# Kernel tuning notes

Hardware: AMD Instinct MI355X
Metric: run time of the kernel (lower is better)

The kernel has to match this reference:

```python
import jax, jax.numpy as jnp
import numpy as np

H, I, E, TOP_K = 2048, 1408, 16, 6
IS = 2816  # shared-expert intermediate = moe_intermediate_size * n_shared_experts
NORM_TOPK_PROB = False


def _silu_and_mul(gate_up):
    # gate_up: [..., 2*I] -> silu(gate) * up, [..., I]
    d = gate_up.shape[-1] // 2
    g, u = gate_up[..., :d], gate_up[..., d:]
    return jax.nn.silu(g) * u


def setup_inputs() -> dict:
    key = jax.random.key(0)
    ks = jax.random.split(key, 6)
    s = 0.02
    return {
        "x": jax.random.normal(ks[0], (1, 2048, H), jnp.float32),
        "gate_w": jax.random.normal(ks[1], (E, H), jnp.float32) * s,
        "w1": jax.random.normal(ks[2], (E, 2 * I, H), jnp.float32) * s,
        "w2": jax.random.normal(ks[3], (E, H, I), jnp.float32) * s,
        "shared_w1": jax.random.normal(ks[4], (2 * IS, H), jnp.float32) * s,
        "shared_w2": jax.random.normal(ks[5], (H, IS), jnp.float32) * s,
    }


def reference(x, gate_w, w1, w2, shared_w1, shared_w2):
    B, S, Hd = x.shape
    xf = x.reshape(-1, Hd)  # [T, H]
    T = xf.shape[0]

    # shared experts (dense MLP over all tokens)
    shared_out = _silu_and_mul(xf @ shared_w1.T) @ shared_w2.T  # [T, H]

    # router: softmax in fp32, then top-k
    logits = xf @ gate_w.T  # [T, E]
    probs = jax.nn.softmax(logits.astype(jnp.float32), axis=-1)
    routing_weights, selected = jax.lax.top_k(probs, TOP_K)  # [T, k]
    if NORM_TOPK_PROB:
        routing_weights = routing_weights / routing_weights.sum(-1, keepdims=True)

    # scatter top-k weights into dense [T, E] combine matrix (fused_moe equivalent)
    combine = jnp.zeros((T, E), jnp.float32).at[
        jnp.arange(T)[:, None], selected
    ].add(routing_weights).astype(x.dtype)

    # expert MLPs, combined with routing weights
    gate_up = jnp.einsum('th,eoh->teo', xf, w1)  # [T, E, 2I]
    act = _silu_and_mul(gate_up)                 # [T, E, I]
    moe_out = jnp.einsum('te,tei,ehi->th', combine, act, w2)  # [T, H]

    return (moe_out + shared_out).reshape(B, S, Hd)
```

## Files before the change

kernel.cpp:

```cpp
#include <hip/hip_runtime.h>
#include <hip/hip_bf16.h>
#include <cstdint>
#include <cstddef>


typedef __bf16 bf16;
typedef __bf16 bf16x8 __attribute__((ext_vector_type(8)));
typedef float  f32x4  __attribute__((ext_vector_type(4)));

constexpr int Hdim  = 2048;
constexpr int Idim  = 1408;
constexpr int NE    = 16;
constexpr int TOPK  = 6;
constexpr int ISdim = 2816;
constexpr int Ttok  = 2048;
constexpr int BMG   = 256;
constexpr int MAX_SLOTS = 16384;

__device__ __forceinline__ void gll16(const void* g, void* l) {
  __builtin_amdgcn_global_load_lds((__attribute__((address_space(1))) void*)(g),
                                   (__attribute__((address_space(3))) void*)(l),
                                   16, 0, 0);
}


__global__ void init_kernel(int* cnt, int* fill, int* tok_of_slot, float* wt_of_slot) {
  int i = blockIdx.x * 256 + threadIdx.x;
  if (i < NE) { cnt[i] = 0; fill[i] = 0; }
  if (i < MAX_SLOTS) { tok_of_slot[i] = -1; wt_of_slot[i] = 0.f; }
}

__global__ void cvt_kernel(const float* __restrict__ src, bf16* __restrict__ dst, int n8) {
  int i = blockIdx.x * 256 + threadIdx.x;
  if (i >= n8) return;
  f32x4 f0 = *(const f32x4*)(src + (size_t)i * 8);
  f32x4 f1 = *(const f32x4*)(src + (size_t)i * 8 + 4);
  bf16x8 v;
#pragma unroll
  for (int j = 0; j < 4; j++) { v[j] = (bf16)f0[j]; v[j + 4] = (bf16)f1[j]; }
  *(bf16x8*)(dst + (size_t)i * 8) = v;
}

__global__ void router_kernel(const float* __restrict__ x, const float* __restrict__ gw,
                              int* __restrict__ sel_e, float* __restrict__ sel_w,
                              int* __restrict__ cnt) {
  int t = blockIdx.x;
  int lane = threadIdx.x;
  const float* xr = x + (size_t)t * Hdim;
  float acc[NE];
#pragma unroll
  for (int e = 0; e < NE; e++) acc[e] = 0.f;
  for (int h = lane; h < Hdim; h += 64) {
    float xv = xr[h];
#pragma unroll
    for (int e = 0; e < NE; e++) acc[e] += xv * gw[e * Hdim + h];
  }
#pragma unroll
  for (int e = 0; e < NE; e++) {
#pragma unroll
    for (int off = 32; off > 0; off >>= 1) acc[e] += __shfl_xor(acc[e], off, 64);
  }
  if (lane == 0) {
    float m = acc[0];
#pragma unroll
    for (int e = 1; e < NE; e++) m = fmaxf(m, acc[e]);
    float p[NE]; float s = 0.f;
#pragma unroll
    for (int e = 0; e < NE; e++) { p[e] = __expf(acc[e] - m); s += p[e]; }
    float inv = 1.f / s;
    bool used[NE];
#pragma unroll
    for (int e = 0; e < NE; e++) used[e] = false;
    for (int k = 0; k < TOPK; k++) {
      int best = 0; float bv = -1.f;
      for (int e = 0; e < NE; e++) if (!used[e] && p[e] > bv) { bv = p[e]; best = e; }
      used[best] = true;
      sel_e[t * TOPK + k] = best;
      sel_w[t * TOPK + k] = bv * inv;
      atomicAdd(&cnt[best], 1);
    }
  }
}

__global__ void scan_kernel(const int* __restrict__ cnt, int* __restrict__ pbase,
                            int* __restrict__ mtiles) {
  if (threadIdx.x == 0 && blockIdx.x == 0) {
    int pb = 0;
    for (int e = 0; e < NE; e++) {
      pbase[e] = pb;
      int mt = (cnt[e] + BMG - 1) / BMG;
      mtiles[e] = mt;
      pb += mt * BMG;
    }
  }
}

__global__ void assign_kernel(const int* __restrict__ sel_e, const float* __restrict__ sel_w,
                              const int* __restrict__ pbase, int* __restrict__ fill,
                              int* __restrict__ tok_of_slot, float* __restrict__ wt_of_slot) {
  int i = blockIdx.x * 256 + threadIdx.x;
  if (i >= Ttok * TOPK) return;
  int t = i / TOPK;
  int e = sel_e[i];
  int pos = atomicAdd(&fill[e], 1);
  int slot = pbase[e] + pos;
  tok_of_slot[slot] = t;
  wt_of_slot[slot] = sel_w[i];
}


template <bool GROUPED, bool BF16B, int BM>
__global__ __launch_bounds__(256, 2)
void gateup_kernel(const bf16* __restrict__ Abase, const void* __restrict__ Wv,
                   bf16* __restrict__ Cact,
                   const int* __restrict__ tok_of_slot, const float* __restrict__ wt_of_slot,
                   const int* __restrict__ pbase, const int* __restrict__ mtiles,
                   int K, int Isz) {
  constexpr int NQ = BM / 64;
  constexpr int WROWS = BM / 4;
  constexpr int NI = WROWS / 16;
  const int e = GROUPED ? blockIdx.z : 0;
  const int mt = blockIdx.y;
  if (GROUPED) { if (mt >= mtiles[e]) return; }
  const int row0 = (GROUPED ? pbase[e] : 0) + mt * BM;
  const int col0 = blockIdx.x * 64;
  const int tid = threadIdx.x;
  const int lane = tid & 63;
  const int wv = tid >> 6;
  const int m16 = lane & 15, quad = lane >> 4;

  __shared__ __align__(16) bf16 ldsA[BM * 32];
  __shared__ __align__(16) bf16 ldsG[64 * 32];
  __shared__ __align__(16) bf16 ldsU[64 * 32];

  const int srow = tid >> 2;
  const int scol = (tid & 3) * 8;

  const bf16* aptr[NQ];
#pragma unroll
  for (int q = 0; q < NQ; q++) {
    int r = row0 + q * 64 + srow;
    int tok = GROUPED ? tok_of_slot[r] : r;
    if (GROUPED && tok < 0) tok = 0;
    aptr[q] = Abase + (size_t)tok * K + scol;
  }

  const bf16* gptrB = nullptr; const bf16* uptrB = nullptr;
  const float* GrowF = nullptr; const float* UrowF = nullptr;
  f32x4 gb0, gb1, ub0, ub1;
  if constexpr (BF16B) {
    const bf16* Wb = (const bf16*)Wv + (size_t)e * 2 * Isz * K;
    gptrB = Wb + (size_t)(col0 + srow) * K + scol;
    uptrB = Wb + (size_t)(Isz + col0 + srow) * K + scol;
  } else {
    const float* Wb = (const float*)Wv + (size_t)e * 2 * Isz * K;
    GrowF = Wb + (size_t)(col0 + srow) * K + scol;
    UrowF = Wb + (size_t)(Isz + col0 + srow) * K + scol;
    gb0 = *(const f32x4*)(GrowF);
    gb1 = *(const f32x4*)(GrowF + 4);
    ub0 = *(const f32x4*)(UrowF);
    ub1 = *(const f32x4*)(UrowF + 4);
  }

  f32x4 accg[NI][4], accu[NI][4];
#pragma unroll
  for (int i = 0; i < NI; i++)
#pragma unroll
    for (int j = 0; j < 4; j++)
#pragma unroll
      for (int r = 0; r < 4; r++) { accg[i][j][r] = 0.f; accu[i][j][r] = 0.f; }

  for (int k0 = 0; k0 < K; k0 += 32) {
    if constexpr (BF16B) {
      gll16(gptrB + k0, &ldsG[tid * 8]);
      gll16(uptrB + k0, &ldsU[tid * 8]);
    } else {
      bf16x8 gv, uv;
#pragma unroll
      for (int j = 0; j < 4; j++) {
        gv[j] = (bf16)gb0[j]; gv[j + 4] = (bf16)gb1[j];
        uv[j] = (bf16)ub0[j]; uv[j + 4] = (bf16)ub1[j];
      }
      *(bf16x8*)(&ldsG[tid * 8]) = gv;
      *(bf16x8*)(&ldsU[tid * 8]) = uv;
      if (k0 + 32 < K) {
        gb0 = *(const f32x4*)(GrowF + k0 + 32);
        gb1 = *(const f32x4*)(GrowF + k0 + 36);
        ub0 = *(const f32x4*)(UrowF + k0 + 32);
        ub1 = *(const f32x4*)(UrowF + k0 + 36);
      }
    }
#pragma unroll
    for (int q = 0; q < NQ; q++) gll16(aptr[q] + k0, &ldsA[q * 2048 + tid * 8]);
    __syncthreads();
    bf16x8 af[NI], gf[4], uf[4];
#pragma unroll
    for (int i = 0; i < NI; i++)
      af[i] = *(const bf16x8*)(&ldsA[(wv * WROWS + i * 16 + m16) * 32 + quad * 8]);
#pragma unroll
    for (int j = 0; j < 4; j++) {
      gf[j] = *(const bf16x8*)(&ldsG[(j * 16 + m16) * 32 + quad * 8]);
      uf[j] = *(const bf16x8*)(&ldsU[(j * 16 + m16) * 32 + quad * 8]);
    }
#pragma unroll
    for (int i = 0; i < NI; i++)
#pragma unroll
      for (int j = 0; j < 4; j++) {
        accg[i][j] = __builtin_amdgcn_mfma_f32_16x16x32_bf16(af[i], gf[j], accg[i][j], 0, 0, 0);
        accu[i][j] = __builtin_amdgcn_mfma_f32_16x16x32_bf16(af[i], uf[j], accu[i][j], 0, 0, 0);
      }
    __syncthreads();
  }

#pragma unroll
  for (int i = 0; i < NI; i++) {
#pragma unroll
    for (int r = 0; r < 4; r++) {
      int grow = row0 + wv * WROWS + i * 16 + quad * 4 + r;
      float scale = 1.f;
      if (GROUPED) scale = wt_of_slot[grow];
#pragma unroll
      for (int j = 0; j < 4; j++) {
        float g = accg[i][j][r];
        float u = accu[i][j][r];
        float a = g * u * scale / (1.f + __expf(-g));
        Cact[(size_t)grow * Isz + (col0 + j * 16 + m16)] = (bf16)a;
      }
    }
  }
}


template <bool GROUPED, bool BF16B, int BM>
__global__ __launch_bounds__(256, 2)
void down_kernel(const bf16* __restrict__ A, const void* __restrict__ Wv,
                 float* __restrict__ out, const int* __restrict__ tok_of_slot,
                 const int* __restrict__ pbase, const int* __restrict__ mtiles, int K) {
  constexpr int NQ = BM / 64;
  constexpr int WROWS = BM / 4;
  constexpr int NI = WROWS / 16;
  const int e = GROUPED ? blockIdx.z : 0;
  const int mt = blockIdx.y;
  if (GROUPED) { if (mt >= mtiles[e]) return; }
  const int row0 = (GROUPED ? pbase[e] : 0) + mt * BM;
  const int col0 = blockIdx.x * 128;
  const int tid = threadIdx.x;
  const int lane = tid & 63;
  const int wv = tid >> 6;
  const int m16 = lane & 15, quad = lane >> 4;

  __shared__ __align__(16) bf16 ldsA[BM * 32];
  __shared__ __align__(16) bf16 ldsB[128 * 32];

  const int srow = tid >> 2;
  const int scol = (tid & 3) * 8;

  const bf16* aptr[NQ];
#pragma unroll
  for (int q = 0; q < NQ; q++)
    aptr[q] = A + (size_t)(row0 + q * 64 + srow) * K + scol;

  const bf16* bptrB[2] = {nullptr, nullptr};
  const float* BrowF[2] = {nullptr, nullptr};
  f32x4 bb[2][2];
  if constexpr (BF16B) {
    const bf16* Wb = (const bf16*)Wv + (size_t)e * Hdim * K;
#pragma unroll
    for (int q = 0; q < 2; q++)
      bptrB[q] = Wb + (size_t)(col0 + q * 64 + srow) * K + scol;
  } else {
    const float* Wb = (const float*)Wv + (size_t)e * Hdim * K;
#pragma unroll
    for (int q = 0; q < 2; q++) {
      BrowF[q] = Wb + (size_t)(col0 + q * 64 + srow) * K + scol;
      bb[q][0] = *(const f32x4*)(BrowF[q]);
      bb[q][1] = *(const f32x4*)(BrowF[q] + 4);
    }
  }

  f32x4 acc[NI][8];
#pragma unroll
  for (int i = 0; i < NI; i++)
#pragma unroll
    for (int j = 0; j < 8; j++)
#pragma unroll
      for (int r = 0; r < 4; r++) acc[i][j][r] = 0.f;

  for (int k0 = 0; k0 < K; k0 += 32) {
    if constexpr (BF16B) {
#pragma unroll
      for (int q = 0; q < 2; q++) gll16(bptrB[q] + k0, &ldsB[q * 2048 + tid * 8]);
    } else {
#pragma unroll
      for (int q = 0; q < 2; q++) {
        bf16x8 bv;
#pragma unroll
        for (int j = 0; j < 4; j++) { bv[j] = (bf16)bb[q][0][j]; bv[j + 4] = (bf16)bb[q][1][j]; }
        *(bf16x8*)(&ldsB[q * 2048 + tid * 8]) = bv;
      }
      if (k0 + 32 < K) {
#pragma unroll
        for (int q = 0; q < 2; q++) {
          bb[q][0] = *(const f32x4*)(BrowF[q] + k0 + 32);
          bb[q][1] = *(const f32x4*)(BrowF[q] + k0 + 36);
        }
      }
    }
#pragma unroll
    for (int q = 0; q < NQ; q++) gll16(aptr[q] + k0, &ldsA[q * 2048 + tid * 8]);
    __syncthreads();
    bf16x8 af[NI], bfr[8];
#pragma unroll
    for (int i = 0; i < NI; i++)
      af[i] = *(const bf16x8*)(&ldsA[(wv * WROWS + i * 16 + m16) * 32 + quad * 8]);
#pragma unroll
    for (int j = 0; j < 8; j++)
      bfr[j] = *(const bf16x8*)(&ldsB[(j * 16 + m16) * 32 + quad * 8]);
#pragma unroll
    for (int i = 0; i < NI; i++)
#pragma unroll
      for (int j = 0; j < 8; j++)
        acc[i][j] = __builtin_amdgcn_mfma_f32_16x16x32_bf16(af[i], bfr[j], acc[i][j], 0, 0, 0);
    __syncthreads();
  }

#pragma unroll
  for (int i = 0; i < NI; i++) {
#pragma unroll
    for (int r = 0; r < 4; r++) {
      int grow = row0 + wv * WROWS + i * 16 + quad * 4 + r;
      int tok;
      if (GROUPED) {
        tok = tok_of_slot[grow];
        if (tok < 0) continue;
      } else {
        tok = grow;
      }
      float* orow = out + (size_t)tok * Hdim;
#pragma unroll
      for (int j = 0; j < 8; j++) {
        int col = col0 + j * 16 + m16;
        if (GROUPED) atomicAdd(orow + col, acc[i][j][r]);
        else orow[col] = acc[i][j][r];
      }
    }
  }
}


extern "C" void kernel_launch(void* const* d_in, const int* in_sizes, int n_in,
                              void* d_out, int out_size, void* d_ws, size_t ws_size,
                              hipStream_t stream) {
  (void)in_sizes; (void)n_in; (void)out_size;
  const float* x   = (const float*)d_in[0];
  const float* gw  = (const float*)d_in[1];
  const float* w1  = (const float*)d_in[2];
  const float* w2  = (const float*)d_in[3];
  const float* sw1 = (const float*)d_in[4];
  const float* sw2 = (const float*)d_in[5];
  float* out = (float*)d_out;

  char* ws = (char*)d_ws;
  size_t off = 0;
  auto alloc = [&](size_t bytes) -> void* {
    void* p = ws + off;
    off += (bytes + 255) & ~(size_t)255;
    return p;
  };
  int*   cnt   = (int*)alloc(NE * 4);
  int*   fill  = (int*)alloc(NE * 4);
  int*   pbase = (int*)alloc(NE * 4);
  int*   mtl   = (int*)alloc(NE * 4);
  int*   sel_e = (int*)alloc((size_t)Ttok * TOPK * 4);
  float* sel_w = (float*)alloc((size_t)Ttok * TOPK * 4);
  int*   tok   = (int*)alloc((size_t)MAX_SLOTS * 4);
  float* wt    = (float*)alloc((size_t)MAX_SLOTS * 4);
  bf16*  xb    = (bf16*)alloc((size_t)Ttok * Hdim * 2);
  bf16*  actx  = (bf16*)alloc((size_t)MAX_SLOTS * Idim * 2);
  bf16*  acts  = (bf16*)alloc((size_t)Ttok * ISdim * 2);

  const size_t n_w1  = (size_t)NE * 2 * Idim * Hdim;
  const size_t n_w2  = (size_t)NE * Hdim * Idim;
  const size_t n_sw1 = (size_t)2 * ISdim * Hdim;
  const size_t n_sw2 = (size_t)Hdim * ISdim;
  size_t off_base = off;
  bf16* w1b  = (bf16*)alloc(n_w1 * 2);
  bf16* w2b  = (bf16*)alloc(n_w2 * 2);
  bf16* sw1b = (bf16*)alloc(n_sw1 * 2);
  bf16* sw2b = (bf16*)alloc(n_sw2 * 2);
  const bool use_bf16w = (off <= ws_size);
  (void)off_base;

  init_kernel<<<(MAX_SLOTS + 255) / 256, 256, 0, stream>>>(cnt, fill, tok, wt);
  cvt_kernel<<<((int)(Ttok * (size_t)Hdim / 8) + 255) / 256, 256, 0, stream>>>(x, xb, Ttok * Hdim / 8);
  router_kernel<<<Ttok, 64, 0, stream>>>(x, gw, sel_e, sel_w, cnt);
  scan_kernel<<<1, 64, 0, stream>>>(cnt, pbase, mtl);
  assign_kernel<<<(Ttok * TOPK + 255) / 256, 256, 0, stream>>>(sel_e, sel_w, pbase, fill, tok, wt);

  if (use_bf16w) {
    cvt_kernel<<<((int)(n_w1 / 8) + 255) / 256, 256, 0, stream>>>(w1, w1b, (int)(n_w1 / 8));
    cvt_kernel<<<((int)(n_w2 / 8) + 255) / 256, 256, 0, stream>>>(w2, w2b, (int)(n_w2 / 8));
    cvt_kernel<<<((int)(n_sw1 / 8) + 255) / 256, 256, 0, stream>>>(sw1, sw1b, (int)(n_sw1 / 8));
    cvt_kernel<<<((int)(n_sw2 / 8) + 255) / 256, 256, 0, stream>>>(sw2, sw2b, (int)(n_sw2 / 8));

    gateup_kernel<true, true, BMG><<<dim3(Idim / 64, Ttok / BMG, NE), 256, 0, stream>>>(
        xb, w1b, actx, tok, wt, pbase, mtl, Hdim, Idim);
    gateup_kernel<false, true, 128><<<dim3(ISdim / 64, Ttok / 128, 1), 256, 0, stream>>>(
        xb, sw1b, acts, nullptr, nullptr, nullptr, nullptr, Hdim, ISdim);
    down_kernel<false, true, 128><<<dim3(Hdim / 128, Ttok / 128, 1), 256, 0, stream>>>(
        acts, sw2b, out, nullptr, nullptr, nullptr, ISdim);
    down_kernel<true, true, BMG><<<dim3(Hdim / 128, Ttok / BMG, NE), 256, 0, stream>>>(
        actx, w2b, out, tok, pbase, mtl, Idim);
  } else {
    gateup_kernel<true, false, BMG><<<dim3(Idim / 64, Ttok / BMG, NE), 256, 0, stream>>>(
        xb, w1, actx, tok, wt, pbase, mtl, Hdim, Idim);
    gateup_kernel<false, false, 128><<<dim3(ISdim / 64, Ttok / 128, 1), 256, 0, stream>>>(
        xb, sw1, acts, nullptr, nullptr, nullptr, nullptr, Hdim, ISdim);
    down_kernel<false, false, 128><<<dim3(Hdim / 128, Ttok / 128, 1), 256, 0, stream>>>(
        acts, sw2, out, nullptr, nullptr, nullptr, ISdim);
    down_kernel<true, false, BMG><<<dim3(Hdim / 128, Ttok / BMG, NE), 256, 0, stream>>>(
        actx, w2, out, tok, pbase, mtl, Idim);
  }
}
```

Before: 1.416 ms.

## Double-buffer GEMM tiles, merge shared and routed launches, replace atomics with combine

Both GEMM kernels now double-buffer their LDS tiles, so the async global-to-LDS load for the next K step is issued before the MFMA work on the current one. Shared-expert and routed-expert work run in a single launch through an extra grid z slice, and the shared expert now uses 256-row tiles. The routed down projection writes per-slot fp32 rows into a buffer that reuses the w1 bf16 storage, and a new combine kernel adds each token's six slot rows into the output. This removes scattered float atomics but adds an extra write and read pass over the slot outputs. The fp32-weight fallback path is dropped, so the code now assumes the workspace always fits the bf16 weights.

```diff
diff --git a/kernel.cpp b/kernel.cpp
--- a/kernel.cpp
+++ b/kernel.cpp
@@ -14,7 +14,7 @@
 constexpr int TOPK  = 6;
 constexpr int ISdim = 2816;
 constexpr int Ttok  = 2048;
-constexpr int BMG   = 256;
+constexpr int BMT   = 256;
 constexpr int MAX_SLOTS = 16384;
 
 __device__ __forceinline__ void gll16(const void* g, void* l) {
@@ -88,50 +88,61 @@
     int pb = 0;
     for (int e = 0; e < NE; e++) {
       pbase[e] = pb;
-      int mt = (cnt[e] + BMG - 1) / BMG;
+      int mt = (cnt[e] + BMT - 1) / BMT;
       mtiles[e] = mt;
-      pb += mt * BMG;
+      pb += mt * BMT;
     }
   }
 }
 
 __global__ void assign_kernel(const int* __restrict__ sel_e, const float* __restrict__ sel_w,
                               const int* __restrict__ pbase, int* __restrict__ fill,
-                              int* __restrict__ tok_of_slot, float* __restrict__ wt_of_slot) {
+                              int* __restrict__ tok_of_slot, float* __restrict__ wt_of_slot,
+                              int* __restrict__ slot_of) {
   int i = blockIdx.x * 256 + threadIdx.x;
   if (i >= Ttok * TOPK) return;
+  int e = sel_e[i];
   int t = i / TOPK;
-  int e = sel_e[i];
   int pos = atomicAdd(&fill[e], 1);
   int slot = pbase[e] + pos;
   tok_of_slot[slot] = t;
   wt_of_slot[slot] = sel_w[i];
-}
-
-
-template <bool GROUPED, bool BF16B, int BM>
+  slot_of[i] = slot;
+}
+
+
+template <int BM>
 __global__ __launch_bounds__(256, 2)
-void gateup_kernel(const bf16* __restrict__ Abase, const void* __restrict__ Wv,
-                   bf16* __restrict__ Cact,
+void gateup_kernel(const bf16* __restrict__ Abase,
+                   const bf16* __restrict__ w1b, const bf16* __restrict__ sw1b,
+                   bf16* __restrict__ actx, bf16* __restrict__ acts,
                    const int* __restrict__ tok_of_slot, const float* __restrict__ wt_of_slot,
-                   const int* __restrict__ pbase, const int* __restrict__ mtiles,
-                   int K, int Isz) {
+                   const int* __restrict__ pbase, const int* __restrict__ mtiles) {
   constexpr int NQ = BM / 64;
   constexpr int WROWS = BM / 4;
   constexpr int NI = WROWS / 16;
-  const int e = GROUPED ? blockIdx.z : 0;
-  const int mt = blockIdx.y;
-  if (GROUPED) { if (mt >= mtiles[e]) return; }
-  const int row0 = (GROUPED ? pbase[e] : 0) + mt * BM;
+  constexpr int K = Hdim;
+  const int z = blockIdx.z;
+  const bool SH = (z == NE);
+  const bf16* Wb; bf16* C; int Isz, row0;
+  if (SH) {
+    Wb = sw1b; C = acts; Isz = ISdim;
+    row0 = blockIdx.y * BM;
+  } else {
+    if (blockIdx.x >= Idim / 64) return;
+    if ((int)blockIdx.y >= mtiles[z]) return;
+    Wb = w1b + (size_t)z * 2 * Idim * Hdim; C = actx; Isz = Idim;
+    row0 = pbase[z] + blockIdx.y * BM;
+  }
   const int col0 = blockIdx.x * 64;
   const int tid = threadIdx.x;
   const int lane = tid & 63;
   const int wv = tid >> 6;
   const int m16 = lane & 15, quad = lane >> 4;
 
-  __shared__ __align__(16) bf16 ldsA[BM * 32];
-  __shared__ __align__(16) bf16 ldsG[64 * 32];
-  __shared__ __align__(16) bf16 ldsU[64 * 32];
+  __shared__ __align__(16) bf16 ldsA[2][BM * 32];
+  __shared__ __align__(16) bf16 ldsG[2][64 * 32];
+  __shared__ __align__(16) bf16 ldsU[2][64 * 32];
 
   const int srow = tid >> 2;
   const int scol = (tid & 3) * 8;
@@ -140,27 +151,12 @@
 #pragma unroll
   for (int q = 0; q < NQ; q++) {
     int r = row0 + q * 64 + srow;
-    int tok = GROUPED ? tok_of_slot[r] : r;
-    if (GROUPED && tok < 0) tok = 0;
+    int tok = SH ? r : tok_of_slot[r];
+    if (tok < 0) tok = 0;
     aptr[q] = Abase + (size_t)tok * K + scol;
   }
-
-  const bf16* gptrB = nullptr; const bf16* uptrB = nullptr;
-  const float* GrowF = nullptr; const float* UrowF = nullptr;
-  f32x4 gb0, gb1, ub0, ub1;
-  if constexpr (BF16B) {
-    const bf16* Wb = (const bf16*)Wv + (size_t)e * 2 * Isz * K;
-    gptrB = Wb + (size_t)(col0 + srow) * K + scol;
-    uptrB = Wb + (size_t)(Isz + col0 + srow) * K + scol;
-  } else {
-    const float* Wb = (const float*)Wv + (size_t)e * 2 * Isz * K;
-    GrowF = Wb + (size_t)(col0 + srow) * K + scol;
-    UrowF = Wb + (size_t)(Isz + col0 + srow) * K + scol;
-    gb0 = *(const f32x4*)(GrowF);
-    gb1 = *(const f32x4*)(GrowF + 4);
-    ub0 = *(const f32x4*)(UrowF);
-    ub1 = *(const f32x4*)(UrowF + 4);
-  }
+  const bf16* gptr = Wb + (size_t)(col0 + srow) * K + scol;
+  const bf16* uptr = Wb + (size_t)(Isz + col0 + srow) * K + scol;
 
   f32x4 accg[NI][4], accu[NI][4];
 #pragma unroll
@@ -170,37 +166,26 @@
 #pragma unroll
       for (int r = 0; r < 4; r++) { accg[i][j][r] = 0.f; accu[i][j][r] = 0.f; }
 
+  auto stage = [&](int b, int k) {
+    gll16(gptr + k, &ldsG[b][tid * 8]);
+    gll16(uptr + k, &ldsU[b][tid * 8]);
+#pragma unroll
+    for (int q = 0; q < NQ; q++) gll16(aptr[q] + k, &ldsA[b][q * 2048 + tid * 8]);
+  };
+
+  stage(0, 0);
+  __syncthreads();
   for (int k0 = 0; k0 < K; k0 += 32) {
-    if constexpr (BF16B) {
-      gll16(gptrB + k0, &ldsG[tid * 8]);
-      gll16(uptrB + k0, &ldsU[tid * 8]);
-    } else {
-      bf16x8 gv, uv;
-#pragma unroll
-      for (int j = 0; j < 4; j++) {
-        gv[j] = (bf16)gb0[j]; gv[j + 4] = (bf16)gb1[j];
-        uv[j] = (bf16)ub0[j]; uv[j + 4] = (bf16)ub1[j];
-      }
-      *(bf16x8*)(&ldsG[tid * 8]) = gv;
-      *(bf16x8*)(&ldsU[tid * 8]) = uv;
-      if (k0 + 32 < K) {
-        gb0 = *(const f32x4*)(GrowF + k0 + 32);
-        gb1 = *(const f32x4*)(GrowF + k0 + 36);
-        ub0 = *(const f32x4*)(UrowF + k0 + 32);
-        ub1 = *(const f32x4*)(UrowF + k0 + 36);
-      }
-    }
-#pragma unroll
-    for (int q = 0; q < NQ; q++) gll16(aptr[q] + k0, &ldsA[q * 2048 + tid * 8]);
-    __syncthreads();
+    const int cur = (k0 >> 5) & 1;
+    if (k0 + 32 < K) stage(cur ^ 1, k0 + 32);
     bf16x8 af[NI], gf[4], uf[4];
 #pragma unroll
     for (int i = 0; i < NI; i++)
-      af[i] = *(const bf16x8*)(&ldsA[(wv * WROWS + i * 16 + m16) * 32 + quad * 8]);
+      af[i] = *(const bf16x8*)(&ldsA[cur][(wv * WROWS + i * 16 + m16) * 32 + quad * 8]);
 #pragma unroll
     for (int j = 0; j < 4; j++) {
-      gf[j] = *(const bf16x8*)(&ldsG[(j * 16 + m16) * 32 + quad * 8]);
-      uf[j] = *(const bf16x8*)(&ldsU[(j * 16 + m16) * 32 + quad * 8]);
+      gf[j] = *(const bf16x8*)(&ldsG[cur][(j * 16 + m16) * 32 + quad * 8]);
+      uf[j] = *(const bf16x8*)(&ldsU[cur][(j * 16 + m16) * 32 + quad * 8]);
     }
 #pragma unroll
     for (int i = 0; i < NI; i++)
@@ -217,40 +202,47 @@
 #pragma unroll
     for (int r = 0; r < 4; r++) {
       int grow = row0 + wv * WROWS + i * 16 + quad * 4 + r;
-      float scale = 1.f;
-      if (GROUPED) scale = wt_of_slot[grow];
+      float scale = SH ? 1.f : wt_of_slot[grow];
 #pragma unroll
       for (int j = 0; j < 4; j++) {
         float g = accg[i][j][r];
         float u = accu[i][j][r];
         float a = g * u * scale / (1.f + __expf(-g));
-        Cact[(size_t)grow * Isz + (col0 + j * 16 + m16)] = (bf16)a;
+        C[(size_t)grow * Isz + (col0 + j * 16 + m16)] = (bf16)a;
       }
     }
   }
 }
 
 
-template <bool GROUPED, bool BF16B, int BM>
+template <int BM>
 __global__ __launch_bounds__(256, 2)
-void down_kernel(const bf16* __restrict__ A, const void* __restrict__ Wv,
-                 float* __restrict__ out, const int* __restrict__ tok_of_slot,
-                 const int* __restrict__ pbase, const int* __restrict__ mtiles, int K) {
+void down_kernel(const bf16* __restrict__ actx, const bf16* __restrict__ acts,
+                 const bf16* __restrict__ w2b, const bf16* __restrict__ sw2b,
+                 float* __restrict__ slot_out, float* __restrict__ out,
+                 const int* __restrict__ pbase, const int* __restrict__ mtiles) {
   constexpr int NQ = BM / 64;
   constexpr int WROWS = BM / 4;
   constexpr int NI = WROWS / 16;
-  const int e = GROUPED ? blockIdx.z : 0;
-  const int mt = blockIdx.y;
-  if (GROUPED) { if (mt >= mtiles[e]) return; }
-  const int row0 = (GROUPED ? pbase[e] : 0) + mt * BM;
+  const int z = blockIdx.z;
+  const bool SH = (z == NE);
+  const bf16* A; const bf16* Wb; float* dst; int K, row0;
+  if (SH) {
+    A = acts; Wb = sw2b; dst = out; K = ISdim;
+    row0 = blockIdx.y * BM;
+  } else {
+    if ((int)blockIdx.y >= mtiles[z]) return;
+    A = actx; Wb = w2b + (size_t)z * Hdim * Idim; dst = slot_out; K = Idim;
+    row0 = pbase[z] + blockIdx.y * BM;
+  }
   const int col0 = blockIdx.x * 128;
   const int tid = threadIdx.x;
   const int lane = tid & 63;
   const int wv = tid >> 6;
   const int m16 = lane & 15, quad = lane >> 4;
 
-  __shared__ __align__(16) bf16 ldsA[BM * 32];
-  __shared__ __align__(16) bf16 ldsB[128 * 32];
+  __shared__ __align__(16) bf16 ldsA[2][BM * 32];
+  __shared__ __align__(16) bf16 ldsB[2][128 * 32];
 
   const int srow = tid >> 2;
   const int scol = (tid & 3) * 8;
@@ -259,24 +251,10 @@
 #pragma unroll
   for (int q = 0; q < NQ; q++)
     aptr[q] = A + (size_t)(row0 + q * 64 + srow) * K + scol;
-
-  const bf16* bptrB[2] = {nullptr, nullptr};
-  const float* BrowF[2] = {nullptr, nullptr};
-  f32x4 bb[2][2];
-  if constexpr (BF16B) {
-    const bf16* Wb = (const bf16*)Wv + (size_t)e * Hdim * K;
-#pragma unroll
-    for (int q = 0; q < 2; q++)
-      bptrB[q] = Wb + (size_t)(col0 + q * 64 + srow) * K + scol;
-  } else {
-    const float* Wb = (const float*)Wv + (size_t)e * Hdim * K;
-#pragma unroll
-    for (int q = 0; q < 2; q++) {
-      BrowF[q] = Wb + (size_t)(col0 + q * 64 + srow) * K + scol;
-      bb[q][0] = *(const f32x4*)(BrowF[q]);
-      bb[q][1] = *(const f32x4*)(BrowF[q] + 4);
-    }
-  }
+  const bf16* bptr[2];
+#pragma unroll
+  for (int q = 0; q < 2; q++)
+    bptr[q] = Wb + (size_t)(col0 + q * 64 + srow) * K + scol;
 
   f32x4 acc[NI][8];
 #pragma unroll
@@ -286,36 +264,25 @@
 #pragma unroll
       for (int r = 0; r < 4; r++) acc[i][j][r] = 0.f;
 
+  auto stage = [&](int b, int k) {
+#pragma unroll
+    for (int q = 0; q < 2; q++) gll16(bptr[q] + k, &ldsB[b][q * 2048 + tid * 8]);
+#pragma unroll
+    for (int q = 0; q < NQ; q++) gll16(aptr[q] + k, &ldsA[b][q * 2048 + tid * 8]);
+  };
+
+  stage(0, 0);
+  __syncthreads();
   for (int k0 = 0; k0 < K; k0 += 32) {
-    if constexpr (BF16B) {
-#pragma unroll
-      for (int q = 0; q < 2; q++) gll16(bptrB[q] + k0, &ldsB[q * 2048 + tid * 8]);
-    } else {
-#pragma unroll
-      for (int q = 0; q < 2; q++) {
-        bf16x8 bv;
-#pragma unroll
-        for (int j = 0; j < 4; j++) { bv[j] = (bf16)bb[q][0][j]; bv[j + 4] = (bf16)bb[q][1][j]; }
-        *(bf16x8*)(&ldsB[q * 2048 + tid * 8]) = bv;
-      }
-      if (k0 + 32 < K) {
-#pragma unroll
-        for (int q = 0; q < 2; q++) {
-          bb[q][0] = *(const f32x4*)(BrowF[q] + k0 + 32);
-          bb[q][1] = *(const f32x4*)(BrowF[q] + k0 + 36);
-        }
-      }
-    }
-#pragma unroll
-    for (int q = 0; q < NQ; q++) gll16(aptr[q] + k0, &ldsA[q * 2048 + tid * 8]);
-    __syncthreads();
+    const int cur = (k0 >> 5) & 1;
+    if (k0 + 32 < K) stage(cur ^ 1, k0 + 32);
     bf16x8 af[NI], bfr[8];
 #pragma unroll
     for (int i = 0; i < NI; i++)
-      af[i] = *(const bf16x8*)(&ldsA[(wv * WROWS + i * 16 + m16) * 32 + quad * 8]);
+      af[i] = *(const bf16x8*)(&ldsA[cur][(wv * WROWS + i * 16 + m16) * 32 + quad * 8]);
 #pragma unroll
     for (int j = 0; j < 8; j++)
-      bfr[j] = *(const bf16x8*)(&ldsB[(j * 16 + m16) * 32 + quad * 8]);
+      bfr[j] = *(const bf16x8*)(&ldsB[cur][(j * 16 + m16) * 32 + quad * 8]);
 #pragma unroll
     for (int i = 0; i < NI; i++)
 #pragma unroll
@@ -329,29 +296,39 @@
 #pragma unroll
     for (int r = 0; r < 4; r++) {
       int grow = row0 + wv * WROWS + i * 16 + quad * 4 + r;
-      int tok;
-      if (GROUPED) {
-        tok = tok_of_slot[grow];
-        if (tok < 0) continue;
-      } else {
-        tok = grow;
-      }
-      float* orow = out + (size_t)tok * Hdim;
-#pragma unroll
-      for (int j = 0; j < 8; j++) {
-        int col = col0 + j * 16 + m16;
-        if (GROUPED) atomicAdd(orow + col, acc[i][j][r]);
-        else orow[col] = acc[i][j][r];
-      }
-    }
-  }
+      float* orow = dst + (size_t)grow * Hdim;
+#pragma unroll
+      for (int j = 0; j < 8; j++) orow[col0 + j * 16 + m16] = acc[i][j][r];
+    }
+  }
+}
+
+
+__global__ void combine_kernel(const float* __restrict__ slot_out,
+                               const int* __restrict__ slot_of,
+                               float* __restrict__ out) {
+  const int t = blockIdx.x;
+  const int c = threadIdx.x * 8;
+  float* op = out + (size_t)t * Hdim + c;
+  f32x4 a0 = *(const f32x4*)op;
+  f32x4 a1 = *(const f32x4*)(op + 4);
+#pragma unroll
+  for (int k = 0; k < TOPK; k++) {
+    int s = slot_of[t * TOPK + k];
+    const float* sp = slot_out + (size_t)s * Hdim + c;
+    f32x4 b0 = *(const f32x4*)sp;
+    f32x4 b1 = *(const f32x4*)(sp + 4);
+    a0 += b0; a1 += b1;
+  }
+  *(f32x4*)op = a0;
+  *(f32x4*)(op + 4) = a1;
 }
 
 
 extern "C" void kernel_launch(void* const* d_in, const int* in_sizes, int n_in,
                               void* d_out, int out_size, void* d_ws, size_t ws_size,
                               hipStream_t stream) {
-  (void)in_sizes; (void)n_in; (void)out_size;
+  (void)in_sizes; (void)n_in; (void)out_size; (void)ws_size;
   const float* x   = (const float*)d_in[0];
   const float* gw  = (const float*)d_in[1];
   const float* w1  = (const float*)d_in[2];
@@ -373,6 +350,7 @@
   int*   mtl   = (int*)alloc(NE * 4);
   int*   sel_e = (int*)alloc((size_t)Ttok * TOPK * 4);
   float* sel_w = (float*)alloc((size_t)Ttok * TOPK * 4);
+  int*   slotf = (int*)alloc((size_t)Ttok * TOPK * 4);
   int*   tok   = (int*)alloc((size_t)MAX_SLOTS * 4);
   float* wt    = (float*)alloc((size_t)MAX_SLOTS * 4);
   bf16*  xb    = (bf16*)alloc((size_t)Ttok * Hdim * 2);
@@ -383,42 +361,26 @@
   const size_t n_w2  = (size_t)NE * Hdim * Idim;
   const size_t n_sw1 = (size_t)2 * ISdim * Hdim;
   const size_t n_sw2 = (size_t)Hdim * ISdim;
-  size_t off_base = off;
   bf16* w1b  = (bf16*)alloc(n_w1 * 2);
   bf16* w2b  = (bf16*)alloc(n_w2 * 2);
   bf16* sw1b = (bf16*)alloc(n_sw1 * 2);
   bf16* sw2b = (bf16*)alloc(n_sw2 * 2);
-  const bool use_bf16w = (off <= ws_size);
-  (void)off_base;
+  float* slot_out = (float*)w1b;
 
   init_kernel<<<(MAX_SLOTS + 255) / 256, 256, 0, stream>>>(cnt, fill, tok, wt);
   cvt_kernel<<<((int)(Ttok * (size_t)Hdim / 8) + 255) / 256, 256, 0, stream>>>(x, xb, Ttok * Hdim / 8);
   router_kernel<<<Ttok, 64, 0, stream>>>(x, gw, sel_e, sel_w, cnt);
   scan_kernel<<<1, 64, 0, stream>>>(cnt, pbase, mtl);
-  assign_kernel<<<(Ttok * TOPK + 255) / 256, 256, 0, stream>>>(sel_e, sel_w, pbase, fill, tok, wt);
-
-  if (use_bf16w) {
-    cvt_kernel<<<((int)(n_w1 / 8) + 255) / 256, 256, 0, stream>>>(w1, w1b, (int)(n_w1 / 8));
-    cvt_kernel<<<((int)(n_w2 / 8) + 255) / 256, 256, 0, stream>>>(w2, w2b, (int)(n_w2 / 8));
-    cvt_kernel<<<((int)(n_sw1 / 8) + 255) / 256, 256, 0, stream>>>(sw1, sw1b, (int)(n_sw1 / 8));
-    cvt_kernel<<<((int)(n_sw2 / 8) + 255) / 256, 256, 0, stream>>>(sw2, sw2b, (int)(n_sw2 / 8));
-
-    gateup_kernel<true, true, BMG><<<dim3(Idim / 64, Ttok / BMG, NE), 256, 0, stream>>>(
-        xb, w1b, actx, tok, wt, pbase, mtl, Hdim, Idim);
-    gateup_kernel<false, true, 128><<<dim3(ISdim / 64, Ttok / 128, 1), 256, 0, stream>>>(
-        xb, sw1b, acts, nullptr, nullptr, nullptr, nullptr, Hdim, ISdim);
-    down_kernel<false, true, 128><<<dim3(Hdim / 128, Ttok / 128, 1), 256, 0, stream>>>(
-        acts, sw2b, out, nullptr, nullptr, nullptr, ISdim);
-    down_kernel<true, true, BMG><<<dim3(Hdim / 128, Ttok / BMG, NE), 256, 0, stream>>>(
-        actx, w2b, out, tok, pbase, mtl, Idim);
-  } else {
-    gateup_kernel<true, false, BMG><<<dim3(Idim / 64, Ttok / BMG, NE), 256, 0, stream>>>(
-        xb, w1, actx, tok, wt, pbase, mtl, Hdim, Idim);
-    gateup_kernel<false, false, 128><<<dim3(ISdim / 64, Ttok / 128, 1), 256, 0, stream>>>(
-        xb, sw1, acts, nullptr, nullptr, nullptr, nullptr, Hdim, ISdim);
-    down_kernel<false, false, 128><<<dim3(Hdim / 128, Ttok / 128, 1), 256, 0, stream>>>(
-        acts, sw2, out, nullptr, nullptr, nullptr, ISdim);
-    down_kernel<true, false, BMG><<<dim3(Hdim / 128, Ttok / BMG, NE), 256, 0, stream>>>(
-        actx, w2, out, tok, pbase, mtl, Idim);
-  }
-}
+  assign_kernel<<<(Ttok * TOPK + 255) / 256, 256, 0, stream>>>(sel_e, sel_w, pbase, fill, tok, wt, slotf);
+
+  cvt_kernel<<<((int)(n_w1 / 8) + 255) / 256, 256, 0, stream>>>(w1, w1b, (int)(n_w1 / 8));
+  cvt_kernel<<<((int)(n_w2 / 8) + 255) / 256, 256, 0, stream>>>(w2, w2b, (int)(n_w2 / 8));
+  cvt_kernel<<<((int)(n_sw1 / 8) + 255) / 256, 256, 0, stream>>>(sw1, sw1b, (int)(n_sw1 / 8));
+  cvt_kernel<<<((int)(n_sw2 / 8) + 255) / 256, 256, 0, stream>>>(sw2, sw2b, (int)(n_sw2 / 8));
+
+  gateup_kernel<BMT><<<dim3(ISdim / 64, Ttok / BMT, NE + 1), 256, 0, stream>>>(
+      xb, w1b, sw1b, actx, acts, tok, wt, pbase, mtl);
+  down_kernel<BMT><<<dim3(Hdim / 128, Ttok / BMT, NE + 1), 256, 0, stream>>>(
+      actx, acts, w2b, sw2b, slot_out, out, pbase, mtl);
+  combine_kernel<<<Ttok, Hdim / 8, 0, stream>>>(slot_out, slotf, out);
+}
```

New measurement: 1.468 ms. +3.7%, slower.
